# Kernel optimization log

Measured on AMD Instinct MI355X. Metric: run time of the kernel, lower is better.

The kernel has to match this reference:

```python
import jax, jax.numpy as jnp
import numpy as np

D_MODEL, D_K, D_V, H = 512, 64, 64, 8
B, NQ, NK = 16, 784, 784
HW = 28  # sqrt(NQ)


def setup_inputs() -> dict:
    key = jax.random.key(0)
    ks = jax.random.split(key, 12)
    std = 0.001  # torch init.normal_(weight, std=0.001)
    return {
        "queries": jax.random.normal(ks[0], (B, NQ, D_MODEL), jnp.float32),
        "keys": jax.random.normal(ks[1], (B, NK, D_MODEL), jnp.float32),
        "values": jax.random.normal(ks[2], (B, NK, D_MODEL), jnp.float32),
        "self_corr": jax.random.normal(ks[3], (B, 1, NQ, NK), jnp.float32),
        # weights stored [in, out] for x @ W
        "Wq": jax.random.normal(ks[4], (D_MODEL, H * D_K), jnp.float32) * std,
        "bq": jnp.zeros((H * D_K,), jnp.float32),
        "Wk": jax.random.normal(ks[5], (D_MODEL, H * D_K), jnp.float32) * std,
        "bk": jnp.zeros((H * D_K,), jnp.float32),
        "Wv": jax.random.normal(ks[6], (D_MODEL, H * D_V), jnp.float32) * std,
        "bv": jnp.zeros((H * D_V,), jnp.float32),
        "Wo": jax.random.normal(ks[7], (H * D_V, D_MODEL), jnp.float32) * std,
        "bo": jnp.zeros((D_MODEL,), jnp.float32),
    }


def reference(queries, keys, values, self_corr, Wq, bq, Wk, bk, Wv, bv, Wo, bo):
    b, nq, cc = queries.shape
    nk = keys.shape[1]
    # projections -> [b, h, n, d]
    q = (queries @ Wq + bq).reshape(b, nq, H, D_K).transpose(0, 2, 1, 3)
    k = (keys @ Wk + bk).reshape(b, nk, H, D_K).transpose(0, 2, 1, 3)
    v = (values @ Wv + bv).reshape(b, nk, H, D_V).transpose(0, 2, 1, 3)
    # scaled scores [b, h, nq, nk]
    att_qk = jnp.einsum("bhqd,bhkd->bhqk", q, k) / np.sqrt(D_K).astype(np.float32)
    enhanced = att_qk + self_corr.reshape(b, -1, nq, nk)  # additive bias (broadcast over heads)
    attn = jax.nn.softmax(enhanced, axis=-1)
    # dropout is identity at inference (reference in eval mode)
    ctx = jnp.einsum("bhqk,bhkd->bhqd", attn, v)
    ctx = ctx.transpose(0, 2, 1, 3).reshape(b, nq, H * D_V)
    out = ctx @ Wo + bo  # [b, nq, d_model]
    hw = int(np.sqrt(nq))
    return out.transpose(0, 2, 1).reshape(b, cc, hw, hw)
```

## Files before the change

### kernel.cpp

```cpp
#include <hip/hip_runtime.h>

#define SZX ((size_t)12544 * 512)
#define WSEG ((size_t)262144)

typedef __attribute__((ext_vector_type(8))) short short8;
typedef __attribute__((ext_vector_type(4))) short short4s;
typedef __attribute__((ext_vector_type(4))) float floatx4;

typedef const __attribute__((address_space(1))) void* gas_cvp;
typedef __attribute__((address_space(3))) void* las_vp;

__device__ __forceinline__ void gl_lds16(const void* g, void* l) {
    __builtin_amdgcn_global_load_lds((gas_cvp)g, (las_vp)l, 16, 0, 0);
}

__device__ __forceinline__ unsigned short f2bf(float f) {
    unsigned int u = __float_as_uint(f);
    u += 0x7fffu + ((u >> 16) & 1u);
    return (unsigned short)(u >> 16);
}

__device__ __forceinline__ short8 lds_read8(const unsigned short* p) {
    short4s a = *(const short4s*)p;
    short4s b = *(const short4s*)(p + 4);
    return __builtin_shufflevector(a, b, 0, 1, 2, 3, 4, 5, 6, 7);
}

#define MFMA16(a, b, c) __builtin_amdgcn_mfma_f32_16x16x32_bf16(a, b, c, 0, 0, 0)

__global__ void cvt3(const float* __restrict__ q, const float* __restrict__ k,
                     const float* __restrict__ v,
                     unsigned short* __restrict__ xq, unsigned short* __restrict__ xk,
                     unsigned short* __restrict__ xv, int which) {
    int sel = blockIdx.y + which;
    const float* in = sel == 0 ? q : sel == 1 ? k : v;
    unsigned short* out = sel == 0 ? xq : sel == 1 ? xk : xv;
    size_t i = ((size_t)blockIdx.x * blockDim.x + threadIdx.x) * 4;
    float4 vv = *(const float4*)(in + i);
    ushort4 o = make_ushort4(f2bf(vv.x), f2bf(vv.y), f2bf(vv.z), f2bf(vv.w));
    *(ushort4*)(out + i) = o;
}

__global__ void transpose_cvt(const float* __restrict__ W0, const float* __restrict__ W1,
                              const float* __restrict__ W2, const float* __restrict__ W3,
                              unsigned short* __restrict__ out) {
    __shared__ float tile[32][33];
    const float* W = blockIdx.z == 0 ? W0 : blockIdx.z == 1 ? W1 : blockIdx.z == 2 ? W2 : W3;
    unsigned short* O = out + (size_t)blockIdx.z * WSEG;
    int x = blockIdx.x * 32 + threadIdx.x;
    int y0 = blockIdx.y * 32;
    for (int k = threadIdx.y; k < 32; k += 8)
        tile[k][threadIdx.x] = W[(size_t)(y0 + k) * 512 + x];
    __syncthreads();
    int xo = blockIdx.y * 32 + threadIdx.x;
    int yo0 = blockIdx.x * 32;
    for (int k = threadIdx.y; k < 32; k += 8)
        O[(size_t)(yo0 + k) * 512 + xo] = f2bf(tile[threadIdx.x][k]);
}

__global__ __launch_bounds__(256) void gemm_qkv(
    const unsigned short* __restrict__ Xq, const unsigned short* __restrict__ Xk,
    const unsigned short* __restrict__ Xv, const unsigned short* __restrict__ Wt,
    const float* __restrict__ bq, const float* __restrict__ bk, const float* __restrict__ bv,
    unsigned short* __restrict__ Qb, unsigned short* __restrict__ Kb,
    unsigned short* __restrict__ Vtb, int zoff)
{
    __shared__ unsigned short Als[128 * 32];
    __shared__ unsigned short Bls[128 * 32];
    int z = blockIdx.z + zoff;
    const unsigned short* X = z == 0 ? Xq : z == 1 ? Xk : Xv;
    const unsigned short* Wz = Wt + (size_t)z * WSEG;
    const float* bias = z == 0 ? bq : z == 1 ? bk : bv;

    int tid = threadIdx.x;
    int lane = tid & 63, wave = tid >> 6;
    int wm = wave & 1, wn = wave >> 1;
    int c16 = lane & 15, g = lane >> 4;
    int tm, tn;
    const unsigned short *Abase, *Bbase;
    if (z < 2) { tm = blockIdx.x; tn = blockIdx.y; Abase = X + (size_t)tm * 128 * 512; Bbase = Wz + (size_t)tn * 128 * 512; }
    else       { tm = blockIdx.y; tn = blockIdx.x; Abase = Wz + (size_t)tm * 128 * 512; Bbase = X + (size_t)tn * 128 * 512; }

    floatx4 acc[4][4];
#pragma unroll
    for (int i = 0; i < 4; i++)
#pragma unroll
        for (int j = 0; j < 4; j++) acc[i][j] = (floatx4){0.f, 0.f, 0.f, 0.f};

    for (int kb = 0; kb < 16; ++kb) {
        int k0 = kb * 32;
#pragma unroll
        for (int rep = 0; rep < 2; ++rep) {
            int slot = rep * 256 + tid;
            int row = slot >> 2, kp = slot & 3;
            gl_lds16(Abase + (size_t)row * 512 + k0 + kp * 8, &Als[slot * 8]);
            gl_lds16(Bbase + (size_t)row * 512 + k0 + kp * 8, &Bls[slot * 8]);
        }
        __syncthreads();
        short8 af[4], bfr[4];
#pragma unroll
        for (int i = 0; i < 4; i++)
            af[i] = *(const short8*)&Als[(wm * 64 + i * 16 + c16) * 32 + g * 8];
#pragma unroll
        for (int j = 0; j < 4; j++)
            bfr[j] = *(const short8*)&Bls[(wn * 64 + j * 16 + c16) * 32 + g * 8];
#pragma unroll
        for (int i = 0; i < 4; i++)
#pragma unroll
            for (int j = 0; j < 4; j++)
                acc[i][j] = MFMA16(af[i], bfr[j], acc[i][j]);
        __syncthreads();
    }

#pragma unroll
    for (int j = 0; j < 4; j++) {
        int n = tn * 128 + wn * 64 + j * 16 + c16;
        int bi = n / 784, nn = n - bi * 784;
        float bvn = (z < 2) ? bias[n] : 0.f;
#pragma unroll
        for (int i = 0; i < 4; i++) {
#pragma unroll
            for (int r4 = 0; r4 < 4; r4++) {
                int m = tm * 128 + wm * 64 + i * 16 + g * 4 + r4;
                float v = acc[i][j][r4] + ((z < 2) ? bvn : bias[m]);
                if (z == 0)      Qb[(size_t)m * 512 + n] = f2bf(v);
                else if (z == 1) Kb[(size_t)m * 512 + n] = f2bf(v);
                else {
                    int h = m >> 6, d = m & 63;
                    Vtb[(((size_t)bi * 8 + h) * 64 + d) * 784 + nn] = f2bf(v);
                }
            }
        }
    }
}

__global__ __launch_bounds__(256) void gemm_out(
    const unsigned short* __restrict__ Wto, const unsigned short* __restrict__ ctx,
    const float* __restrict__ bo, float* __restrict__ out)
{
    __shared__ unsigned short Als[64 * 32];
    __shared__ unsigned short Bls[128 * 32];
    int tid = threadIdx.x;
    int lane = tid & 63, wn = tid >> 6;
    int c16 = lane & 15, g = lane >> 4;
    int tm = blockIdx.x, tn = blockIdx.y;

    const unsigned short* Abase = Wto + (size_t)tm * 64 * 512;
    const unsigned short* Bbase = ctx + (size_t)tn * 128 * 512;

    floatx4 acc[4][2];
#pragma unroll
    for (int i = 0; i < 4; i++)
#pragma unroll
        for (int j = 0; j < 2; j++) acc[i][j] = (floatx4){0.f, 0.f, 0.f, 0.f};

    for (int kb = 0; kb < 16; ++kb) {
        int k0 = kb * 32;
        {
            int row = tid >> 2, kp = tid & 3;
            gl_lds16(Abase + (size_t)row * 512 + k0 + kp * 8, &Als[tid * 8]);
        }
#pragma unroll
        for (int rep = 0; rep < 2; ++rep) {
            int slot = rep * 256 + tid;
            int row = slot >> 2, kp = slot & 3;
            gl_lds16(Bbase + (size_t)row * 512 + k0 + kp * 8, &Bls[slot * 8]);
        }
        __syncthreads();
        short8 af[4], bfr[2];
#pragma unroll
        for (int i = 0; i < 4; i++)
            af[i] = *(const short8*)&Als[(i * 16 + c16) * 32 + g * 8];
#pragma unroll
        for (int j = 0; j < 2; j++)
            bfr[j] = *(const short8*)&Bls[(wn * 32 + j * 16 + c16) * 32 + g * 8];
#pragma unroll
        for (int i = 0; i < 4; i++)
#pragma unroll
            for (int j = 0; j < 2; j++)
                acc[i][j] = MFMA16(af[i], bfr[j], acc[i][j]);
        __syncthreads();
    }

#pragma unroll
    for (int j = 0; j < 2; j++) {
        int n = tn * 128 + wn * 32 + j * 16 + c16;
        int bi = n / 784, q = n - bi * 784;
#pragma unroll
        for (int i = 0; i < 4; i++) {
#pragma unroll
            for (int r4 = 0; r4 < 4; r4++) {
                int m = tm * 64 + i * 16 + g * 4 + r4;
                out[((size_t)bi * 512 + m) * 784 + q] = acc[i][j][r4] + bo[m];
            }
        }
    }
}

__global__ __launch_bounds__(256) void attn_kernel(
    const unsigned short* __restrict__ Qb,
    const unsigned short* __restrict__ Kb,
    const unsigned short* __restrict__ Vtb,
    const float* __restrict__ corr,
    unsigned short* __restrict__ ctx)
{
    __shared__ unsigned short Plds[2][4][2][16][68];
    int b = blockIdx.x, qt = blockIdx.y, hh = blockIdx.z;
    int tid = threadIdx.x;
    int lane = tid & 63, w = tid >> 6;
    int h = hh * 4 + w;
    int c16 = lane & 15, g = lane >> 4;
    int q0 = qt * 32;

    short8 aq[2][2];
#pragma unroll
    for (int u = 0; u < 2; ++u) {
        int row = q0 + u * 16 + c16; row = row < 784 ? row : 783;
        const unsigned short* qp = Qb + (size_t)(b * 784 + row) * 512 + h * 64 + g * 8;
        aq[u][0] = *(const short8*)qp;
        aq[u][1] = *(const short8*)(qp + 32);
    }

    floatx4 o[2][4];
    float l[2][4];
#pragma unroll
    for (int u = 0; u < 2; ++u)
#pragma unroll
        for (int nt = 0; nt < 4; nt++) { o[u][nt] = (floatx4){0.f, 0.f, 0.f, 0.f}; l[u][nt] = 0.f; }

    const float* corrb = corr + (size_t)b * 784 * 784;
    int crow[2][4];
#pragma unroll
    for (int u = 0; u < 2; ++u)
#pragma unroll
        for (int r = 0; r < 4; ++r) {
            int rr = q0 + u * 16 + g * 4 + r; rr = rr < 784 ? rr : 783;
            crow[u][r] = rr * 784;
        }

    const unsigned short* Vh = Vtb + ((size_t)(b * 8 + h)) * 64 * 784;
    const unsigned short* Kh = Kb + (size_t)b * 784 * 512 + h * 64;

    for (int it = 0; it < 13; ++it) {
        int k0 = it * 64;
        floatx4 s[2][4];
#pragma unroll
        for (int t = 0; t < 4; ++t) {
            int key = k0 + t * 16 + c16; key = key < 784 ? key : 783;
            const unsigned short* kp = Kh + (size_t)key * 512 + g * 8;
            short8 k0f = *(const short8*)kp;
            short8 k1f = *(const short8*)(kp + 32);
#pragma unroll
            for (int u = 0; u < 2; ++u) {
                floatx4 zz = (floatx4){0.f, 0.f, 0.f, 0.f};
                zz = MFMA16(aq[u][0], k0f, zz);
                zz = MFMA16(aq[u][1], k1f, zz);
                s[u][t] = zz;
            }
        }
        unsigned short* pbase = &Plds[it & 1][w][0][0][0];
#pragma unroll
        for (int u = 0; u < 2; ++u)
#pragma unroll
            for (int t = 0; t < 4; ++t) {
                int key = k0 + t * 16 + c16;
                bool valid = key < 784;
                int kc = valid ? key : 783;
#pragma unroll
                for (int r = 0; r < 4; ++r) {
                    float cv = corrb[crow[u][r] + kc];
                    float sv = fmaf(s[u][t][r], 0.125f, cv);
                    float pv = valid ? __expf(sv) : 0.f;
                    l[u][r] += pv;
                    pbase[(u * 16 + g * 4 + r) * 68 + t * 16 + c16] = f2bf(pv);
                }
            }
#pragma unroll
        for (int u = 0; u < 2; ++u) {
            const unsigned short* pr = &Plds[it & 1][w][u][c16][0];
            short8 pa0 = lds_read8(pr + g * 8);
            short8 pa1 = lds_read8(pr + 32 + g * 8);
#pragma unroll
            for (int nt = 0; nt < 4; ++nt) {
                int d = nt * 16 + c16;
                const unsigned short* vp = Vh + (size_t)d * 784 + k0 + g * 8;
                short8 v0 = *(const short8*)vp;
                short8 v1 = *(const short8*)(vp + 32);
                o[u][nt] = MFMA16(pa0, v0, o[u][nt]);
                o[u][nt] = MFMA16(pa1, v1, o[u][nt]);
            }
        }
    }

#pragma unroll
    for (int u = 0; u < 2; ++u)
#pragma unroll
        for (int r = 0; r < 4; ++r) {
            float lv = l[u][r];
            lv += __shfl_xor(lv, 1);
            lv += __shfl_xor(lv, 2);
            lv += __shfl_xor(lv, 4);
            lv += __shfl_xor(lv, 8);
            l[u][r] = 1.0f / lv;
        }
#pragma unroll
    for (int u = 0; u < 2; ++u)
#pragma unroll
        for (int r = 0; r < 4; ++r) {
            int row = q0 + u * 16 + g * 4 + r;
            if (row < 784) {
#pragma unroll
                for (int nt = 0; nt < 4; ++nt)
                    ctx[(size_t)(b * 784 + row) * 512 + h * 64 + nt * 16 + c16] =
                        f2bf(o[u][nt][r] * l[u][r]);
            }
        }
}

extern "C" void kernel_launch(void* const* d_in, const int* in_sizes, int n_in,
                              void* d_out, int out_size, void* d_ws, size_t ws_size,
                              hipStream_t stream) {
    (void)in_sizes; (void)n_in; (void)out_size;
    const float* queries = (const float*)d_in[0];
    const float* keys    = (const float*)d_in[1];
    const float* values  = (const float*)d_in[2];
    const float* corr    = (const float*)d_in[3];
    const float* Wq = (const float*)d_in[4];
    const float* bq = (const float*)d_in[5];
    const float* Wk = (const float*)d_in[6];
    const float* bk = (const float*)d_in[7];
    const float* Wv = (const float*)d_in[8];
    const float* bv = (const float*)d_in[9];
    const float* Wo = (const float*)d_in[10];
    const float* bo = (const float*)d_in[11];

    size_t need = (6 * SZX + 4 * WSEG) * 2;
    if (ws_size >= need) {
        unsigned short* Xq  = (unsigned short*)d_ws;
        unsigned short* Xk  = Xq + SZX;
        unsigned short* Xv  = Xk + SZX;
        unsigned short* Qb  = Xv + SZX;
        unsigned short* Kb  = Qb + SZX;
        unsigned short* Vtb = Kb + SZX;
        unsigned short* Wt  = Vtb + SZX;

        transpose_cvt<<<dim3(16, 16, 4), dim3(32, 8), 0, stream>>>(Wq, Wk, Wv, Wo, Wt);
        cvt3<<<dim3(6272, 3), 256, 0, stream>>>(queries, keys, values, Xq, Xk, Xv, 0);
        gemm_qkv<<<dim3(98, 4, 3), 256, 0, stream>>>(Xq, Xk, Xv, Wt, bq, bk, bv, Qb, Kb, Vtb, 0);
        attn_kernel<<<dim3(16, 25, 2), 256, 0, stream>>>(Qb, Kb, Vtb, corr, Xq);
        gemm_out<<<dim3(8, 98), 256, 0, stream>>>(Wt + 3 * WSEG, Xq, bo, (float*)d_out);
    } else {
        unsigned short* X   = (unsigned short*)d_ws;
        unsigned short* Qb  = X + SZX;
        unsigned short* Kb  = Qb + SZX;
        unsigned short* Vtb = Kb + SZX;
        unsigned short* Wt  = Vtb + SZX;

        transpose_cvt<<<dim3(16, 16, 4), dim3(32, 8), 0, stream>>>(Wq, Wk, Wv, Wo, Wt);
        for (int z = 0; z < 3; ++z) {
            cvt3<<<dim3(6272, 1), 256, 0, stream>>>(queries, keys, values, X, X, X, z);
            gemm_qkv<<<dim3(98, 4, 1), 256, 0, stream>>>(X, X, X, Wt, bq, bk, bv, Qb, Kb, Vtb, z);
        }
        attn_kernel<<<dim3(16, 25, 2), 256, 0, stream>>>(Qb, Kb, Vtb, corr, X);
        gemm_out<<<dim3(8, 98), 256, 0, stream>>>(Wt + 3 * WSEG, X, bo, (float*)d_out);
    }
}
```

Measured before the change: 326.1 us.

## Transpose QK MFMA so correlation bias loads as float4 and P stores vectorize

Swaps the MFMA operand order in the score computation so each lane holds four consecutive keys for one query row instead of four rows for one key. The self-correlation bias can then be read as one float4 per tile, prefetched at the top of each iteration, and P can be written to LDS as packed 8-byte stores. The row-sum reduction is rewritten to match the new lane layout. It also adds s_setprio around the MFMA groups. The float4 loads must stay correctly aligned and masked at the 784 boundary.

```diff
diff --git a/kernel.cpp b/kernel.cpp
--- a/kernel.cpp
+++ b/kernel.cpp
@@ -222,27 +222,38 @@
     }
 
     floatx4 o[2][4];
-    float l[2][4];
-#pragma unroll
-    for (int u = 0; u < 2; ++u)
-#pragma unroll
-        for (int nt = 0; nt < 4; nt++) { o[u][nt] = (floatx4){0.f, 0.f, 0.f, 0.f}; l[u][nt] = 0.f; }
+    float l[2];
+#pragma unroll
+    for (int u = 0; u < 2; ++u) {
+        l[u] = 0.f;
+#pragma unroll
+        for (int nt = 0; nt < 4; nt++) o[u][nt] = (floatx4){0.f, 0.f, 0.f, 0.f};
+    }
 
     const float* corrb = corr + (size_t)b * 784 * 784;
-    int crow[2][4];
-#pragma unroll
-    for (int u = 0; u < 2; ++u)
-#pragma unroll
-        for (int r = 0; r < 4; ++r) {
-            int rr = q0 + u * 16 + g * 4 + r; rr = rr < 784 ? rr : 783;
-            crow[u][r] = rr * 784;
-        }
+    size_t crow[2];
+#pragma unroll
+    for (int u = 0; u < 2; ++u) {
+        int qr = q0 + u * 16 + c16; qr = qr < 784 ? qr : 783;
+        crow[u] = (size_t)qr * 784;
+    }
 
     const unsigned short* Vh = Vtb + ((size_t)(b * 8 + h)) * 64 * 784;
     const unsigned short* Kh = Kb + (size_t)b * 784 * 512 + h * 64;
 
     for (int it = 0; it < 13; ++it) {
         int k0 = it * 64;
+
+        float4 cc[2][4];
+#pragma unroll
+        for (int u = 0; u < 2; ++u)
+#pragma unroll
+            for (int t = 0; t < 4; ++t) {
+                int kc = k0 + t * 16 + g * 4;
+                kc = kc < 780 ? kc : 780;
+                cc[u][t] = *(const float4*)(corrb + crow[u] + kc);
+            }
+
         floatx4 s[2][4];
 #pragma unroll
         for (int t = 0; t < 4; ++t) {
@@ -250,31 +261,35 @@
             const unsigned short* kp = Kh + (size_t)key * 512 + g * 8;
             short8 k0f = *(const short8*)kp;
             short8 k1f = *(const short8*)(kp + 32);
+            __builtin_amdgcn_s_setprio(1);
 #pragma unroll
             for (int u = 0; u < 2; ++u) {
                 floatx4 zz = (floatx4){0.f, 0.f, 0.f, 0.f};
-                zz = MFMA16(aq[u][0], k0f, zz);
-                zz = MFMA16(aq[u][1], k1f, zz);
+                zz = MFMA16(k0f, aq[u][0], zz);
+                zz = MFMA16(k1f, aq[u][1], zz);
                 s[u][t] = zz;
             }
-        }
-        unsigned short* pbase = &Plds[it & 1][w][0][0][0];
+            __builtin_amdgcn_s_setprio(0);
+        }
+
 #pragma unroll
         for (int u = 0; u < 2; ++u)
 #pragma unroll
             for (int t = 0; t < 4; ++t) {
-                int key = k0 + t * 16 + c16;
-                bool valid = key < 784;
-                int kc = valid ? key : 783;
+                int kb2 = k0 + t * 16 + g * 4;
+                const float* cp = (const float*)&cc[u][t];
+                float pvv[4];
 #pragma unroll
                 for (int r = 0; r < 4; ++r) {
-                    float cv = corrb[crow[u][r] + kc];
-                    float sv = fmaf(s[u][t][r], 0.125f, cv);
-                    float pv = valid ? __expf(sv) : 0.f;
-                    l[u][r] += pv;
-                    pbase[(u * 16 + g * 4 + r) * 68 + t * 16 + c16] = f2bf(pv);
+                    float sv = fmaf(s[u][t][r], 0.125f, cp[r]);
+                    pvv[r] = (kb2 + r < 784) ? __expf(sv) : 0.f;
+                    l[u] += pvv[r];
                 }
-            }
+                unsigned int w0 = (unsigned)f2bf(pvv[0]) | ((unsigned)f2bf(pvv[1]) << 16);
+                unsigned int w1 = (unsigned)f2bf(pvv[2]) | ((unsigned)f2bf(pvv[3]) << 16);
+                *(uint2*)&Plds[it & 1][w][u][c16][t * 16 + g * 4] = make_uint2(w0, w1);
+            }
+
 #pragma unroll
         for (int u = 0; u < 2; ++u) {
             const unsigned short* pr = &Plds[it & 1][w][u][c16][0];
@@ -286,33 +301,33 @@
                 const unsigned short* vp = Vh + (size_t)d * 784 + k0 + g * 8;
                 short8 v0 = *(const short8*)vp;
                 short8 v1 = *(const short8*)(vp + 32);
+                __builtin_amdgcn_s_setprio(1);
                 o[u][nt] = MFMA16(pa0, v0, o[u][nt]);
                 o[u][nt] = MFMA16(pa1, v1, o[u][nt]);
-            }
-        }
-    }
-
-#pragma unroll
-    for (int u = 0; u < 2; ++u)
-#pragma unroll
-        for (int r = 0; r < 4; ++r) {
-            float lv = l[u][r];
-            lv += __shfl_xor(lv, 1);
-            lv += __shfl_xor(lv, 2);
-            lv += __shfl_xor(lv, 4);
-            lv += __shfl_xor(lv, 8);
-            l[u][r] = 1.0f / lv;
-        }
+                __builtin_amdgcn_s_setprio(0);
+            }
+        }
+    }
+
+    float linv[2];
+#pragma unroll
+    for (int u = 0; u < 2; ++u) {
+        float lv = l[u];
+        lv += __shfl_xor(lv, 16);
+        lv += __shfl_xor(lv, 32);
+        linv[u] = 1.0f / lv;
+    }
 #pragma unroll
     for (int u = 0; u < 2; ++u)
 #pragma unroll
         for (int r = 0; r < 4; ++r) {
             int row = q0 + u * 16 + g * 4 + r;
+            float li = __shfl(linv[u], g * 4 + r);
             if (row < 784) {
 #pragma unroll
                 for (int nt = 0; nt < 4; ++nt)
                     ctx[(size_t)(b * 784 + row) * 512 + h * 64 + nt * 16 + c16] =
-                        f2bf(o[u][nt][r] * l[u][r]);
+                        f2bf(o[u][nt][r] * li);
             }
         }
 }
```

Result: slower. 350.1 us (+7.4%).

## Prefetch correlation bias tiles into LDS with async global-to-LDS loads

Applied to the files above, without the earlier changes.

The attention kernel used to read the fp32 self-correlation bias straight from global memory as scattered 4-byte loads inside the softmax loop. It now stages each wave's 32x64 bias tile into LDS with 16-byte global_load_lds transfers, issued one key-tile ahead so the load overlaps the PV MFMA work. The P staging buffer goes from double to single buffering to make room for the new LDS space. A full vmcnt(0) wait before the softmax section serializes all outstanding vector loads. The last tile relies on clamped columns that are masked as invalid keys.

```diff
diff --git a/kernel.cpp b/kernel.cpp
--- a/kernel.cpp
+++ b/kernel.cpp
@@ -204,7 +204,8 @@
     const float* __restrict__ corr,
     unsigned short* __restrict__ ctx)
 {
-    __shared__ unsigned short Plds[2][4][2][16][68];
+    __shared__ unsigned short Plds[4][2][16][68];
+    __shared__ float Clds[4][32][64];
     int b = blockIdx.x, qt = blockIdx.y, hh = blockIdx.z;
     int tid = threadIdx.x;
     int lane = tid & 63, w = tid >> 6;
@@ -229,20 +230,32 @@
         for (int nt = 0; nt < 4; nt++) { o[u][nt] = (floatx4){0.f, 0.f, 0.f, 0.f}; l[u][nt] = 0.f; }
 
     const float* corrb = corr + (size_t)b * 784 * 784;
-    int crow[2][4];
-#pragma unroll
-    for (int u = 0; u < 2; ++u)
-#pragma unroll
-        for (int r = 0; r < 4; ++r) {
-            int rr = q0 + u * 16 + g * 4 + r; rr = rr < 784 ? rr : 783;
-            crow[u][r] = rr * 784;
-        }
+
+    int jr = lane >> 4;
+    int jc = lane & 15;
+    size_t crow_dma[8];
+#pragma unroll
+    for (int j = 0; j < 8; ++j) {
+        int row = q0 + j * 4 + jr; row = row < 784 ? row : 783;
+        crow_dma[j] = (size_t)row * 784;
+    }
 
     const unsigned short* Vh = Vtb + ((size_t)(b * 8 + h)) * 64 * 784;
     const unsigned short* Kh = Kb + (size_t)b * 784 * 512 + h * 64;
 
+    auto corr_dma = [&](int it) {
+        int kstart = it * 64 + jc * 4;
+        kstart = kstart < 780 ? kstart : 780;
+#pragma unroll
+        for (int j = 0; j < 8; ++j)
+            gl_lds16(corrb + crow_dma[j] + kstart, &Clds[w][j * 4 + jr][jc * 4]);
+    };
+
+    corr_dma(0);
+
     for (int it = 0; it < 13; ++it) {
         int k0 = it * 64;
+
         floatx4 s[2][4];
 #pragma unroll
         for (int t = 0; t < 4; ++t) {
@@ -258,26 +271,32 @@
                 s[u][t] = zz;
             }
         }
-        unsigned short* pbase = &Plds[it & 1][w][0][0][0];
+
+        asm volatile("s_waitcnt vmcnt(0)" ::: "memory");
+        __builtin_amdgcn_sched_barrier(0);
+
+        unsigned short* pbase = &Plds[w][0][0][0];
 #pragma unroll
         for (int u = 0; u < 2; ++u)
 #pragma unroll
             for (int t = 0; t < 4; ++t) {
                 int key = k0 + t * 16 + c16;
                 bool valid = key < 784;
-                int kc = valid ? key : 783;
 #pragma unroll
                 for (int r = 0; r < 4; ++r) {
-                    float cv = corrb[crow[u][r] + kc];
+                    float cv = Clds[w][u * 16 + g * 4 + r][t * 16 + c16];
                     float sv = fmaf(s[u][t][r], 0.125f, cv);
                     float pv = valid ? __expf(sv) : 0.f;
                     l[u][r] += pv;
                     pbase[(u * 16 + g * 4 + r) * 68 + t * 16 + c16] = f2bf(pv);
                 }
             }
+
+        if (it < 12) corr_dma(it + 1);
+
 #pragma unroll
         for (int u = 0; u < 2; ++u) {
-            const unsigned short* pr = &Plds[it & 1][w][u][c16][0];
+            const unsigned short* pr = &Plds[w][u][c16][0];
             short8 pa0 = lds_read8(pr + g * 8);
             short8 pa1 = lds_read8(pr + 32 + g * 8);
 #pragma unroll
```

New measurement: 333.2 us. 1.02x slower.

## Fuse fp32-to-bf16 input conversion into the QKV projection GEMM

Applied to the files above, without the earlier changes.

Removes the standalone conversion kernel that wrote bf16 copies of queries, keys and values. The QKV GEMM now streams fp32 activations directly into a swizzled LDS tile and converts them to bf16 while building MFMA fragments. The V path swaps operand roles in the MFMA instead of swapping the loaded tiles. This removes a full extra write and read of the activations, but doubles the LDS bytes and global traffic per X tile and adds conversion ALU work inside the GEMM loop.

```diff
diff --git a/kernel.cpp b/kernel.cpp
--- a/kernel.cpp
+++ b/kernel.cpp
@@ -20,6 +20,15 @@
     return (unsigned short)(u >> 16);
 }
 
+__device__ __forceinline__ short8 cvt8(floatx4 a, floatx4 b) {
+    short8 r;
+    r[0] = (short)f2bf(a[0]); r[1] = (short)f2bf(a[1]);
+    r[2] = (short)f2bf(a[2]); r[3] = (short)f2bf(a[3]);
+    r[4] = (short)f2bf(b[0]); r[5] = (short)f2bf(b[1]);
+    r[6] = (short)f2bf(b[2]); r[7] = (short)f2bf(b[3]);
+    return r;
+}
+
 __device__ __forceinline__ short8 lds_read8(const unsigned short* p) {
     short4s a = *(const short4s*)p;
     short4s b = *(const short4s*)(p + 4);
@@ -27,19 +36,6 @@
 }
 
 #define MFMA16(a, b, c) __builtin_amdgcn_mfma_f32_16x16x32_bf16(a, b, c, 0, 0, 0)
-
-__global__ void cvt3(const float* __restrict__ q, const float* __restrict__ k,
-                     const float* __restrict__ v,
-                     unsigned short* __restrict__ xq, unsigned short* __restrict__ xk,
-                     unsigned short* __restrict__ xv, int which) {
-    int sel = blockIdx.y + which;
-    const float* in = sel == 0 ? q : sel == 1 ? k : v;
-    unsigned short* out = sel == 0 ? xq : sel == 1 ? xk : xv;
-    size_t i = ((size_t)blockIdx.x * blockDim.x + threadIdx.x) * 4;
-    float4 vv = *(const float4*)(in + i);
-    ushort4 o = make_ushort4(f2bf(vv.x), f2bf(vv.y), f2bf(vv.z), f2bf(vv.w));
-    *(ushort4*)(out + i) = o;
-}
 
 __global__ void transpose_cvt(const float* __restrict__ W0, const float* __restrict__ W1,
                               const float* __restrict__ W2, const float* __restrict__ W3,
@@ -59,16 +55,16 @@
 }
 
 __global__ __launch_bounds__(256) void gemm_qkv(
-    const unsigned short* __restrict__ Xq, const unsigned short* __restrict__ Xk,
-    const unsigned short* __restrict__ Xv, const unsigned short* __restrict__ Wt,
+    const float* __restrict__ Xq, const float* __restrict__ Xk,
+    const float* __restrict__ Xv, const unsigned short* __restrict__ Wt,
     const float* __restrict__ bq, const float* __restrict__ bk, const float* __restrict__ bv,
     unsigned short* __restrict__ Qb, unsigned short* __restrict__ Kb,
-    unsigned short* __restrict__ Vtb, int zoff)
+    unsigned short* __restrict__ Vtb)
 {
-    __shared__ unsigned short Als[128 * 32];
-    __shared__ unsigned short Bls[128 * 32];
-    int z = blockIdx.z + zoff;
-    const unsigned short* X = z == 0 ? Xq : z == 1 ? Xk : Xv;
+    __shared__ float Xls[128 * 32];
+    __shared__ unsigned short Wls[128 * 32];
+    int z = blockIdx.z;
+    const float* X = z == 0 ? Xq : z == 1 ? Xk : Xv;
     const unsigned short* Wz = Wt + (size_t)z * WSEG;
     const float* bias = z == 0 ? bq : z == 1 ? bk : bv;
 
@@ -76,10 +72,13 @@
     int lane = tid & 63, wave = tid >> 6;
     int wm = wave & 1, wn = wave >> 1;
     int c16 = lane & 15, g = lane >> 4;
-    int tm, tn;
-    const unsigned short *Abase, *Bbase;
-    if (z < 2) { tm = blockIdx.x; tn = blockIdx.y; Abase = X + (size_t)tm * 128 * 512; Bbase = Wz + (size_t)tn * 128 * 512; }
-    else       { tm = blockIdx.y; tn = blockIdx.x; Abase = Wz + (size_t)tm * 128 * 512; Bbase = X + (size_t)tn * 128 * 512; }
+
+    const float* Xbase = X + (size_t)blockIdx.x * 128 * 512;
+    const unsigned short* Wbase = Wz + (size_t)blockIdx.y * 128 * 512;
+    int tm = (z < 2) ? blockIdx.x : blockIdx.y;
+    int tn = (z < 2) ? blockIdx.y : blockIdx.x;
+    int wx = (z < 2) ? wm : wn;
+    int ww = (z < 2) ? wn : wm;
 
     floatx4 acc[4][4];
 #pragma unroll
@@ -89,26 +88,47 @@
 
     for (int kb = 0; kb < 16; ++kb) {
         int k0 = kb * 32;
+#pragma unroll
+        for (int rep = 0; rep < 4; ++rep) {
+            int slot = rep * 256 + tid;
+            int row = slot >> 3, kp = slot & 7;
+            int src = kp ^ (row & 7);
+            gl_lds16(Xbase + (size_t)row * 512 + k0 + src * 4, &Xls[slot * 4]);
+        }
 #pragma unroll
         for (int rep = 0; rep < 2; ++rep) {
             int slot = rep * 256 + tid;
             int row = slot >> 2, kp = slot & 3;
-            gl_lds16(Abase + (size_t)row * 512 + k0 + kp * 8, &Als[slot * 8]);
-            gl_lds16(Bbase + (size_t)row * 512 + k0 + kp * 8, &Bls[slot * 8]);
+            gl_lds16(Wbase + (size_t)row * 512 + k0 + kp * 8, &Wls[slot * 8]);
         }
         __syncthreads();
-        short8 af[4], bfr[4];
-#pragma unroll
-        for (int i = 0; i < 4; i++)
-            af[i] = *(const short8*)&Als[(wm * 64 + i * 16 + c16) * 32 + g * 8];
+
+        short8 xf[4], wf[4];
+#pragma unroll
+        for (int i = 0; i < 4; i++) {
+            int row = wx * 64 + i * 16 + c16;
+            int sw = row & 7;
+            floatx4 a = *(const floatx4*)&Xls[row * 32 + ((2 * g + 0) ^ sw) * 4];
+            floatx4 b2 = *(const floatx4*)&Xls[row * 32 + ((2 * g + 1) ^ sw) * 4];
+            xf[i] = cvt8(a, b2);
+        }
 #pragma unroll
         for (int j = 0; j < 4; j++)
-            bfr[j] = *(const short8*)&Bls[(wn * 64 + j * 16 + c16) * 32 + g * 8];
-#pragma unroll
-        for (int i = 0; i < 4; i++)
-#pragma unroll
-            for (int j = 0; j < 4; j++)
-                acc[i][j] = MFMA16(af[i], bfr[j], acc[i][j]);
+            wf[j] = *(const short8*)&Wls[(ww * 64 + j * 16 + c16) * 32 + g * 8];
+
+        if (z < 2) {
+#pragma unroll
+            for (int i = 0; i < 4; i++)
+#pragma unroll
+                for (int j = 0; j < 4; j++)
+                    acc[i][j] = MFMA16(xf[i], wf[j], acc[i][j]);
+        } else {
+#pragma unroll
+            for (int i = 0; i < 4; i++)
+#pragma unroll
+                for (int j = 0; j < 4; j++)
+                    acc[i][j] = MFMA16(wf[i], xf[j], acc[i][j]);
+        }
         __syncthreads();
     }
 
@@ -320,7 +340,7 @@
 extern "C" void kernel_launch(void* const* d_in, const int* in_sizes, int n_in,
                               void* d_out, int out_size, void* d_ws, size_t ws_size,
                               hipStream_t stream) {
-    (void)in_sizes; (void)n_in; (void)out_size;
+    (void)in_sizes; (void)n_in; (void)out_size; (void)ws_size;
     const float* queries = (const float*)d_in[0];
     const float* keys    = (const float*)d_in[1];
     const float* values  = (const float*)d_in[2];
@@ -334,34 +354,15 @@
     const float* Wo = (const float*)d_in[10];
     const float* bo = (const float*)d_in[11];
 
-    size_t need = (6 * SZX + 4 * WSEG) * 2;
-    if (ws_size >= need) {
-        unsigned short* Xq  = (unsigned short*)d_ws;
-        unsigned short* Xk  = Xq + SZX;
-        unsigned short* Xv  = Xk + SZX;
-        unsigned short* Qb  = Xv + SZX;
-        unsigned short* Kb  = Qb + SZX;
-        unsigned short* Vtb = Kb + SZX;
-        unsigned short* Wt  = Vtb + SZX;
-
-        transpose_cvt<<<dim3(16, 16, 4), dim3(32, 8), 0, stream>>>(Wq, Wk, Wv, Wo, Wt);
-        cvt3<<<dim3(6272, 3), 256, 0, stream>>>(queries, keys, values, Xq, Xk, Xv, 0);
-        gemm_qkv<<<dim3(98, 4, 3), 256, 0, stream>>>(Xq, Xk, Xv, Wt, bq, bk, bv, Qb, Kb, Vtb, 0);
-        attn_kernel<<<dim3(16, 25, 2), 256, 0, stream>>>(Qb, Kb, Vtb, corr, Xq);
-        gemm_out<<<dim3(8, 98), 256, 0, stream>>>(Wt + 3 * WSEG, Xq, bo, (float*)d_out);
-    } else {
-        unsigned short* X   = (unsigned short*)d_ws;
-        unsigned short* Qb  = X + SZX;
-        unsigned short* Kb  = Qb + SZX;
-        unsigned short* Vtb = Kb + SZX;
-        unsigned short* Wt  = Vtb + SZX;
-
-        transpose_cvt<<<dim3(16, 16, 4), dim3(32, 8), 0, stream>>>(Wq, Wk, Wv, Wo, Wt);
-        for (int z = 0; z < 3; ++z) {
-            cvt3<<<dim3(6272, 1), 256, 0, stream>>>(queries, keys, values, X, X, X, z);
-            gemm_qkv<<<dim3(98, 4, 1), 256, 0, stream>>>(X, X, X, Wt, bq, bk, bv, Qb, Kb, Vtb, z);
-        }
-        attn_kernel<<<dim3(16, 25, 2), 256, 0, stream>>>(Qb, Kb, Vtb, corr, X);
-        gemm_out<<<dim3(8, 98), 256, 0, stream>>>(Wt + 3 * WSEG, X, bo, (float*)d_out);
-    }
-}
+    unsigned short* Qb  = (unsigned short*)d_ws;
+    unsigned short* Kb  = Qb + SZX;
+    unsigned short* Vtb = Kb + SZX;
+    unsigned short* ctx = Vtb + SZX;
+    unsigned short* Wt  = ctx + SZX;
+
+    transpose_cvt<<<dim3(16, 16, 4), dim3(32, 8), 0, stream>>>(Wq, Wk, Wv, Wo, Wt);
+    gemm_qkv<<<dim3(98, 4, 3), 256, 0, stream>>>(queries, keys, values, Wt,
+                                                 bq, bk, bv, Qb, Kb, Vtb);
+    attn_kernel<<<dim3(16, 25, 2), 256, 0, stream>>>(Qb, Kb, Vtb, corr, ctx);
+    gemm_out<<<dim3(8, 98), 256, 0, stream>>>(Wt + 3 * WSEG, ctx, bo, (float*)d_out);
+}
```

After: 335.2 us. +2.8%, slower.
